# Performance work log

Hardware: AMD Instinct MI355X
Metric: run time of the kernel (lower is better)

Reference implementation:

```python
import jax, jax.numpy as jnp
import numpy as np

B, C, H, W = 8, 384, 128, 128
WSZ = 8          # window size
DH = 32          # dim per head
HEADS = C // DH  # 12
INNER = HEADS * DH
EPS = 1e-5


def setup_inputs() -> dict:
    key = jax.random.key(0)
    ks = jax.random.split(key, 6)
    x = jax.random.normal(ks[0], (B, C, H, W), jnp.float32)
    skip = jax.random.normal(ks[1], (B, C, H, W), jnp.float32)
    # LayerNorm affine params (shape (1, C, 1, 1) in torch; store as (C,))
    g_q = jnp.ones((C,), jnp.float32)
    b_q = jnp.zeros((C,), jnp.float32)
    g_kv = jnp.ones((C,), jnp.float32)
    b_kv = jnp.zeros((C,), jnp.float32)
    # 1x1 conv weights: [out_channels, in_channels]
    Wq = jax.random.normal(ks[2], (INNER, C), jnp.float32) * 0.05
    Wkv = jax.random.normal(ks[3], (2 * INNER, C), jnp.float32) * 0.05
    Wout = jax.random.normal(ks[4], (C, INNER), jnp.float32) * 0.05
    bout = jax.random.normal(ks[5], (C,), jnp.float32) * 0.05
    return dict(x=x, skip=skip, g_q=g_q, b_q=b_q, g_kv=g_kv, b_kv=b_kv,
                Wq=Wq, Wkv=Wkv, Wout=Wout, bout=bout)


def _channel_ln(x, g, b):
    # LayerNorm over channel dim (axis=1), biased variance
    mean = jnp.mean(x, axis=1, keepdims=True)
    var = jnp.mean((x - mean) ** 2, axis=1, keepdims=True)
    return (x - mean) / jnp.sqrt(var + EPS) * g[None, :, None, None] + b[None, :, None, None]


def _to_windows(x):
    # [B, C, H, W] -> [B*nh*nw, C, wsz, wsz]
    b, c, h, w = x.shape
    nh, nw = h // WSZ, w // WSZ
    x = x.reshape(b, c, nh, WSZ, nw, WSZ).transpose(0, 2, 4, 1, 3, 5)
    return x.reshape(b * nh * nw, c, WSZ, WSZ)


def _from_windows(x, b, h, w):
    # [B*nh*nw, C, wsz, wsz] -> [B, C, H, W]
    nh, nw = h // WSZ, w // WSZ
    c = x.shape[1]
    x = x.reshape(b, nh, nw, c, WSZ, WSZ).transpose(0, 3, 1, 4, 2, 5)
    return x.reshape(b, c, h, w)


def _split_heads(t):
    # [Bw, heads*dh, wsz, wsz] -> [Bw, heads, wsz*wsz, dh]
    bw = t.shape[0]
    t = t.reshape(bw, HEADS, DH, WSZ * WSZ)
    return t.transpose(0, 1, 3, 2)


def reference(x, skip, g_q, b_q, g_kv, b_kv, Wq, Wkv, Wout, bout):
    b, _, h, w = x.shape
    xn = _to_windows(_channel_ln(x, g_q, b_q))
    skn = _to_windows(_channel_ln(skip, g_kv, b_kv))
    # 1x1 convs as channel GEMMs
    q = jnp.einsum('oc,bcxy->boxy', Wq, xn)
    kv = jnp.einsum('oc,bcxy->boxy', Wkv, skn)
    k, v = kv[:, :INNER], kv[:, INNER:]
    q, k, v = _split_heads(q), _split_heads(k), _split_heads(v)
    scale = DH ** -0.5
    attn = jax.nn.softmax(jnp.einsum('bhqd,bhkd->bhqk', q, k) * scale, axis=-1)
    out = jnp.einsum('bhqk,bhkd->bhqd', attn, v)
    # [Bw, heads, S, dh] -> [Bw, inner, wsz, wsz]
    out = out.transpose(0, 1, 3, 2).reshape(-1, INNER, WSZ, WSZ)
    out = jnp.einsum('oc,bcxy->boxy', Wout, out) + bout[None, :, None, None]
    return _from_windows(out, b, h, w)
```

## Files before the change

### kernel.cpp

```cpp
#include <hip/hip_runtime.h>
#include <stdint.h>

typedef __attribute__((ext_vector_type(4))) float f32x4;
typedef __attribute__((ext_vector_type(8))) short s16x8;
typedef unsigned int u32;
typedef unsigned short u16;

#define DEVFN static __device__ __forceinline__

constexpr int C = 384;
constexpr int WIMG = 128;
constexpr int HW = 128 * 128;
constexpr float EPS = 1e-5f;
constexpr float QSCALE = 0.17677669529663687f;

constexpr int R1 = 0;
constexpr int R2 = 49152;
constexpr int R3 = 98304;
constexpr int PR = 147456;
constexpr int LDS_BYTES = 163840;

DEVFN u16 f2bf(float f) {
  union { float f; u32 u; } v; v.f = f;
  u32 r = v.u + 0x7fffu + ((v.u >> 16) & 1u);
  return (u16)(r >> 16);
}
DEVFN f32x4 MFMA(s16x8 a, s16x8 b, f32x4 c) {
  return __builtin_amdgcn_mfma_f32_16x16x32_bf16(a, b, c, 0, 0, 0);
}
DEVFN int adr768(int base, int row, int b) { return base + row * 768 + (b ^ ((row & 7) << 4)); }
DEVFN int adr128(int base, int row, int b) { return base + row * 128 + (b ^ ((row & 7) << 4)); }

__global__ void cvt_bf16_kernel(const float* __restrict__ src, u16* __restrict__ dst, int n) {
  int i = (blockIdx.x * blockDim.x + threadIdx.x) * 4;
  if (i + 3 < n) {
    f32x4 v = *(const f32x4*)(src + i);
    u32* d = (u32*)(dst + i);
    d[0] = (u32)f2bf(v[0]) | ((u32)f2bf(v[1]) << 16);
    d[1] = (u32)f2bf(v[2]) | ((u32)f2bf(v[3]) << 16);
  }
}

__global__ void fold_ln_weights(const float* __restrict__ Wq, const float* __restrict__ Wkv,
                                const float* __restrict__ gq, const float* __restrict__ bq,
                                const float* __restrict__ gkv, const float* __restrict__ bkv,
                                u16* __restrict__ wqb, u16* __restrict__ wkb, u16* __restrict__ wvb,
                                float* __restrict__ sg_all, float* __restrict__ sb_all) {
  int r = blockIdx.x * 4 + (threadIdx.x >> 6);
  int lane = threadIdx.x & 63;
  const float* src; const float* g; const float* b; u16* dst; float scale;
  if (r < 384) { src = Wq + (size_t)r * C; g = gq; b = bq; dst = wqb + (size_t)r * C; scale = QSCALE; }
  else {
    src = Wkv + (size_t)(r - 384) * C; g = gkv; b = bkv; scale = 1.f;
    dst = (r < 768) ? wkb + (size_t)(r - 384) * C : wvb + (size_t)(r - 768) * C;
  }
  float sg = 0.f, sb = 0.f;
#pragma unroll
  for (int i = 0; i < 6; ++i) {
    int c = lane + i * 64;
    float wv = src[c], gg = g[c];
    sg += wv * gg; sb += wv * b[c];
    dst[c] = f2bf(wv * gg * scale);
  }
#pragma unroll
  for (int m = 1; m < 64; m <<= 1) { sg += __shfl_xor(sg, m); sb += __shfl_xor(sb, m); }
  if (lane == 0) { sg_all[r] = sg * scale; sb_all[r] = sb * scale; }
}

__launch_bounds__(512, 2)
__global__ void fused_win_attn(
    const float* __restrict__ x, const float* __restrict__ skip,
    const u16* __restrict__ wqb, const u16* __restrict__ wkb,
    const u16* __restrict__ wvb, const u16* __restrict__ wob,
    const float* __restrict__ sg_all, const float* __restrict__ sb_all,
    const float* __restrict__ bout, float* __restrict__ out) {
  extern __shared__ char smem[];
  const int tid = threadIdx.x;
  const int lane = tid & 63;
  const int w = tid >> 6;
  const int l15 = lane & 15;
  const int lg = lane >> 4;
  const int kco = lg * 8;

  const int bid = blockIdx.x;
  const int win = (bid & 7) * 256 + (bid >> 3);
  const int bimg = win >> 8;
  const int Y0 = ((win >> 4) & 15) * 8;
  const int X0 = (win & 15) * 8;
  const size_t img_off = (size_t)bimg * C * HW;

  const f32x4 fzero = {0.f, 0.f, 0.f, 0.f};

  float* red = (float*)(smem + PR);
  float* stats_x = (float*)(smem + PR + 4096);
  float* stats_s = (float*)(smem + PR + 4608);

  const int p = tid & 63;
  const int g8 = tid >> 6;
  const int yy = p >> 3, xx = p & 7;

  for (int tt = 0; tt < 2; ++tt) {
    const float* src = tt ? skip : x;
    const int RB = tt ? R2 : R1;
    const float* gb = src + img_off + (size_t)(Y0 + yy) * WIMG + X0 + xx;
    float s = 0.f, q = 0.f;
#pragma unroll
    for (int i = 0; i < 24; ++i) {
      int c0 = g8 * 48 + i * 2;
      float v0 = gb[(size_t)c0 * HW];
      float v1 = gb[(size_t)c0 * HW + HW];
      s += v0 + v1; q += v0 * v0 + v1 * v1;
      *(u32*)(smem + adr768(RB, p, c0 * 2)) = (u32)f2bf(v0) | ((u32)f2bf(v1) << 16);
    }
    red[tid * 2] = s; red[tid * 2 + 1] = q;
    __syncthreads();
    if (tid < 64) {
      float sm = 0.f, sq = 0.f;
#pragma unroll
      for (int gg = 0; gg < 8; ++gg) { sm += red[(gg * 64 + tid) * 2]; sq += red[(gg * 64 + tid) * 2 + 1]; }
      float mean = sm * (1.f / 384.f);
      float var = sq * (1.f / 384.f) - mean * mean;
      float* st = tt ? stats_s : stats_x;
      st[tid * 2] = mean; st[tid * 2 + 1] = 1.f / sqrtf(var + EPS);
    }
    __syncthreads();
  }

  {
    f32x4 acc[3][4];
#pragma unroll
    for (int nn = 0; nn < 3; ++nn)
#pragma unroll
      for (int m = 0; m < 4; ++m) acc[nn][m] = fzero;
#pragma unroll
    for (int k = 0; k < 12; ++k) {
      s16x8 A[4];
#pragma unroll
      for (int m = 0; m < 4; ++m)
        A[m] = *(const s16x8*)(smem + adr768(R2, m * 16 + l15, (k * 32 + kco) * 2));
#pragma unroll
      for (int nn = 0; nn < 3; ++nn) {
        s16x8 B = *(const s16x8*)(wkb + (size_t)((3 * w + nn) * 16 + l15) * C + k * 32 + kco);
#pragma unroll
        for (int m = 0; m < 4; ++m) acc[nn][m] = MFMA(A[m], B, acc[nn][m]);
      }
    }
#pragma unroll
    for (int nn = 0; nn < 3; ++nn) {
      int o = (3 * w + nn) * 16 + l15;
      float sg = sg_all[384 + o], sb = sb_all[384 + o];
#pragma unroll
      for (int m = 0; m < 4; ++m)
#pragma unroll
        for (int j = 0; j < 4; ++j) {
          int tok = m * 16 + lg * 4 + j;
          float mn = stats_s[tok * 2], rs = stats_s[tok * 2 + 1];
          *(u16*)(smem + adr768(R3, tok, o * 2)) = f2bf(rs * acc[nn][m][j] - rs * mn * sg + sb);
        }
    }
  }

  f32x4 accV[3][4];
  {
#pragma unroll
    for (int mm = 0; mm < 3; ++mm)
#pragma unroll
      for (int n = 0; n < 4; ++n) accV[mm][n] = fzero;
#pragma unroll
    for (int k = 0; k < 12; ++k) {
      s16x8 Bv[4];
#pragma unroll
      for (int n = 0; n < 4; ++n)
        Bv[n] = *(const s16x8*)(smem + adr768(R2, n * 16 + l15, (k * 32 + kco) * 2));
#pragma unroll
      for (int mm = 0; mm < 3; ++mm) {
        s16x8 A = *(const s16x8*)(wvb + (size_t)((3 * w + mm) * 16 + l15) * C + k * 32 + kco);
#pragma unroll
        for (int n = 0; n < 4; ++n) accV[mm][n] = MFMA(A, Bv[n], accV[mm][n]);
      }
    }
  }

  f32x4 accQ[3][4];
  {
#pragma unroll
    for (int nn = 0; nn < 3; ++nn)
#pragma unroll
      for (int m = 0; m < 4; ++m) accQ[nn][m] = fzero;
#pragma unroll
    for (int k = 0; k < 12; ++k) {
      s16x8 A[4];
#pragma unroll
      for (int m = 0; m < 4; ++m)
        A[m] = *(const s16x8*)(smem + adr768(R1, m * 16 + l15, (k * 32 + kco) * 2));
#pragma unroll
      for (int nn = 0; nn < 3; ++nn) {
        s16x8 B = *(const s16x8*)(wqb + (size_t)((3 * w + nn) * 16 + l15) * C + k * 32 + kco);
#pragma unroll
        for (int m = 0; m < 4; ++m) accQ[nn][m] = MFMA(A[m], B, accQ[nn][m]);
      }
    }
  }
  __syncthreads();

  {
#pragma unroll
    for (int mm = 0; mm < 3; ++mm)
#pragma unroll
      for (int j = 0; j < 4; ++j) {
        int dh = (3 * w + mm) * 16 + lg * 4 + j;
        float sg = sg_all[768 + dh], sb = sb_all[768 + dh];
#pragma unroll
        for (int n = 0; n < 4; ++n) {
          int tok = n * 16 + l15;
          float mn = stats_s[tok * 2], rs = stats_s[tok * 2 + 1];
          *(u16*)(smem + adr128(R2, dh, tok * 2)) = f2bf(rs * accV[mm][n][j] - rs * mn * sg + sb);
        }
      }
#pragma unroll
    for (int nn = 0; nn < 3; ++nn) {
      int o = (3 * w + nn) * 16 + l15;
      float sg = sg_all[o], sb = sb_all[o];
#pragma unroll
      for (int m = 0; m < 4; ++m)
#pragma unroll
        for (int j = 0; j < 4; ++j) {
          int tok = m * 16 + lg * 4 + j;
          float mn = stats_x[tok * 2], rs = stats_x[tok * 2 + 1];
          *(u16*)(smem + adr768(R1, tok, o * 2)) = f2bf(rs * accQ[nn][m][j] - rs * mn * sg + sb);
        }
    }
  }
  __syncthreads();

  const int qt = w & 3;
  const int hh = w >> 2;
  char* strip = smem + PR + w * 2048;
  const int swzq = (l15 & 7) << 4;

  s16x8 oA[6];

#pragma unroll
  for (int hloc = 0; hloc < 6; ++hloc) {
    const int h = hh * 6 + hloc;
    s16x8 bq = *(const s16x8*)(smem + adr768(R1, qt * 16 + l15, h * 64 + lg * 16));
    f32x4 sc[4];
#pragma unroll
    for (int m = 0; m < 4; ++m) {
      s16x8 ak = *(const s16x8*)(smem + adr768(R3, m * 16 + l15, h * 64 + lg * 16));
      sc[m] = MFMA(ak, bq, fzero);
    }
    float mx = sc[0][0];
#pragma unroll
    for (int m = 0; m < 4; ++m)
#pragma unroll
      for (int j = 0; j < 4; ++j) mx = fmaxf(mx, sc[m][j]);
    mx = fmaxf(mx, __shfl_xor(mx, 16));
    mx = fmaxf(mx, __shfl_xor(mx, 32));
    float ex[4][4];
    float sum = 0.f;
#pragma unroll
    for (int m = 0; m < 4; ++m)
#pragma unroll
      for (int j = 0; j < 4; ++j) { float e = __expf(sc[m][j] - mx); ex[m][j] = e; sum += e; }
    sum += __shfl_xor(sum, 16);
    sum += __shfl_xor(sum, 32);
    float inv = 1.0f / sum;
#pragma unroll
    for (int m = 0; m < 4; ++m)
#pragma unroll
      for (int j2 = 0; j2 < 2; ++j2) {
        u32 pk = (u32)f2bf(ex[m][2 * j2] * inv) | ((u32)f2bf(ex[m][2 * j2 + 1] * inv) << 16);
        *(u32*)(strip + l15 * 128 + ((m * 32 + lg * 8 + j2 * 4) ^ swzq)) = pk;
      }
    f32x4 ov[2] = {fzero, fzero};
#pragma unroll
    for (int ks = 0; ks < 2; ++ks) {
      s16x8 ap = *(const s16x8*)(strip + l15 * 128 + ((ks * 64 + lg * 16) ^ swzq));
#pragma unroll
      for (int n = 0; n < 2; ++n) {
        s16x8 bv = *(const s16x8*)(smem + adr128(R2, h * 32 + n * 16 + l15, ks * 64 + lg * 16));
        ov[n] = MFMA(ap, bv, ov[n]);
      }
    }
#pragma unroll
    for (int n = 0; n < 2; ++n)
#pragma unroll
      for (int j = 0; j < 4; ++j) {
        int row = lg * 4 + j;
        *(u16*)(strip + row * 128 + ((n * 32 + l15 * 2) ^ ((row & 7) << 4))) = f2bf(ov[n][j]);
      }
    oA[hloc] = *(const s16x8*)(strip + l15 * 128 + ((lg * 16) ^ swzq));
  }

#pragma unroll
  for (int hloc = 0; hloc < 6; ++hloc)
    *(s16x8*)(smem + adr768(R1, qt * 16 + l15, (hh * 6 + hloc) * 64 + lg * 16)) = oA[hloc];
  __syncthreads();

  f32x4 outacc[3][4];
#pragma unroll
  for (int nn = 0; nn < 3; ++nn)
#pragma unroll
    for (int m = 0; m < 4; ++m) outacc[nn][m] = fzero;
#pragma unroll
  for (int k = 0; k < 12; ++k) {
    s16x8 A[4];
#pragma unroll
    for (int m = 0; m < 4; ++m)
      A[m] = *(const s16x8*)(smem + adr768(R1, m * 16 + l15, (k * 32 + kco) * 2));
#pragma unroll
    for (int nn = 0; nn < 3; ++nn) {
      s16x8 B = *(const s16x8*)(wob + (size_t)((3 * w + nn) * 16 + l15) * C + k * 32 + kco);
#pragma unroll
      for (int m = 0; m < 4; ++m) outacc[nn][m] = MFMA(A[m], B, outacc[nn][m]);
    }
  }
  __syncthreads();

  float* outf = (float*)smem;
#pragma unroll
  for (int nn = 0; nn < 3; ++nn) {
    int o = (3 * w + nn) * 16 + l15;
    float bo = bout[o];
#pragma unroll
    for (int m = 0; m < 4; ++m)
#pragma unroll
      for (int j = 0; j < 4; ++j)
        outf[(m * 16 + lg * 4 + j) * 385 + o] = outacc[nn][m][j] + bo;
  }
  __syncthreads();
  {
    float* ob = out + img_off + (size_t)(Y0 + yy) * WIMG + X0 + xx;
#pragma unroll
    for (int i = 0; i < 48; ++i) {
      int c = g8 * 48 + i;
      ob[(size_t)c * HW] = outf[p * 385 + c];
    }
  }
}

extern "C" void kernel_launch(void* const* d_in, const int* in_sizes, int n_in,
                              void* d_out, int out_size, void* d_ws, size_t ws_size,
                              hipStream_t stream) {
  const float* x    = (const float*)d_in[0];
  const float* skip = (const float*)d_in[1];
  const float* gq   = (const float*)d_in[2];
  const float* bq   = (const float*)d_in[3];
  const float* gkv  = (const float*)d_in[4];
  const float* bkv  = (const float*)d_in[5];
  const float* Wq   = (const float*)d_in[6];
  const float* Wkv  = (const float*)d_in[7];
  const float* Wout = (const float*)d_in[8];
  const float* bout = (const float*)d_in[9];
  float* out = (float*)d_out;

  char* ws = (char*)d_ws;
  u16* wqb = (u16*)(ws);
  u16* wkb = (u16*)(ws + 294912);
  u16* wvb = (u16*)(ws + 589824);
  u16* wob = (u16*)(ws + 884736);
  float* sg_all = (float*)(ws + 1179648);
  float* sb_all = (float*)(ws + 1184256);

  hipFuncSetAttribute((const void*)fused_win_attn,
                      hipFuncAttributeMaxDynamicSharedMemorySize, LDS_BYTES);

  fold_ln_weights<<<288, 256, 0, stream>>>(Wq, Wkv, gq, bq, gkv, bkv, wqb, wkb, wvb, sg_all, sb_all);
  cvt_bf16_kernel<<<144, 256, 0, stream>>>(Wout, wob, 147456);

  fused_win_attn<<<2048, 512, LDS_BYTES, stream>>>(
      x, skip, wqb, wkb, wvb, wob, sg_all, sb_all, bout, out);
}
```

Measured before the change: 599.1 us.

## Double block to 1024 threads and redistribute K/Q/V/attention/output work across 16 waves

The fused window-attention kernel now runs 16 waves per block instead of 8. The K and Q projections run concurrently on separate wave halves, and the V projection and output GEMM are split over token halves. Attention now handles 3 heads per wave, with a smaller per-wave strip, and writes its output directly into the Q region instead of staging it through registers. The aim is more latency hiding and per-block parallelism, at the cost of extra barriers and possibly lower occupancy, since the LDS budget still limits how many blocks fit per CU.

```diff
diff --git a/kernel.cpp b/kernel.cpp
--- a/kernel.cpp
+++ b/kernel.cpp
@@ -67,7 +67,7 @@
   if (lane == 0) { sg_all[r] = sg * scale; sb_all[r] = sb * scale; }
 }
 
-__launch_bounds__(512, 2)
+__launch_bounds__(1024, 4)
 __global__ void fused_win_attn(
     const float* __restrict__ x, const float* __restrict__ skip,
     const u16* __restrict__ wqb, const u16* __restrict__ wkb,
@@ -79,8 +79,8 @@
   const int lane = tid & 63;
   const int w = tid >> 6;
   const int l15 = lane & 15;
-  const int lg = lane >> 4;
-  const int kco = lg * 8;
+  const int g = lane >> 4;
+  const int kco = g * 8;
 
   const int bid = blockIdx.x;
   const int win = (bid & 7) * 256 + (bid >> 3);
@@ -92,11 +92,10 @@
   const f32x4 fzero = {0.f, 0.f, 0.f, 0.f};
 
   float* red = (float*)(smem + PR);
-  float* stats_x = (float*)(smem + PR + 4096);
-  float* stats_s = (float*)(smem + PR + 4608);
-
-  const int p = tid & 63;
-  const int g8 = tid >> 6;
+  float* stats_x = (float*)(smem + PR + 8192);
+  float* stats_s = (float*)(smem + PR + 8704);
+
+  const int p = lane;
   const int yy = p >> 3, xx = p & 7;
 
   for (int tt = 0; tt < 2; ++tt) {
@@ -105,8 +104,8 @@
     const float* gb = src + img_off + (size_t)(Y0 + yy) * WIMG + X0 + xx;
     float s = 0.f, q = 0.f;
 #pragma unroll
-    for (int i = 0; i < 24; ++i) {
-      int c0 = g8 * 48 + i * 2;
+    for (int i = 0; i < 12; ++i) {
+      int c0 = w * 24 + i * 2;
       float v0 = gb[(size_t)c0 * HW];
       float v1 = gb[(size_t)c0 * HW + HW];
       s += v0 + v1; q += v0 * v0 + v1 * v1;
@@ -117,7 +116,7 @@
     if (tid < 64) {
       float sm = 0.f, sq = 0.f;
 #pragma unroll
-      for (int gg = 0; gg < 8; ++gg) { sm += red[(gg * 64 + tid) * 2]; sq += red[(gg * 64 + tid) * 2 + 1]; }
+      for (int gg = 0; gg < 16; ++gg) { sm += red[(gg * 64 + tid) * 2]; sq += red[(gg * 64 + tid) * 2 + 1]; }
       float mean = sm * (1.f / 384.f);
       float var = sq * (1.f / 384.f) - mean * mean;
       float* st = tt ? stats_s : stats_x;
@@ -126,7 +125,8 @@
     __syncthreads();
   }
 
-  {
+  f32x4 accQ[3][4];
+  if (w < 8) {
     f32x4 acc[3][4];
 #pragma unroll
     for (int nn = 0; nn < 3; ++nn)
@@ -137,7 +137,7 @@
       s16x8 A[4];
 #pragma unroll
       for (int m = 0; m < 4; ++m)
-        A[m] = *(const s16x8*)(smem + adr768(R2, m * 16 + l15, (k * 32 + kco) * 2));
+        A[m] = *(const s16x8*)(smem + adr768(R2, m * 16 + l15, k * 64 + g * 16));
 #pragma unroll
       for (int nn = 0; nn < 3; ++nn) {
         s16x8 B = *(const s16x8*)(wkb + (size_t)((3 * w + nn) * 16 + l15) * C + k * 32 + kco);
@@ -153,36 +153,13 @@
       for (int m = 0; m < 4; ++m)
 #pragma unroll
         for (int j = 0; j < 4; ++j) {
-          int tok = m * 16 + lg * 4 + j;
+          int tok = m * 16 + g * 4 + j;
           float mn = stats_s[tok * 2], rs = stats_s[tok * 2 + 1];
           *(u16*)(smem + adr768(R3, tok, o * 2)) = f2bf(rs * acc[nn][m][j] - rs * mn * sg + sb);
         }
     }
-  }
-
-  f32x4 accV[3][4];
-  {
-#pragma unroll
-    for (int mm = 0; mm < 3; ++mm)
-#pragma unroll
-      for (int n = 0; n < 4; ++n) accV[mm][n] = fzero;
-#pragma unroll
-    for (int k = 0; k < 12; ++k) {
-      s16x8 Bv[4];
-#pragma unroll
-      for (int n = 0; n < 4; ++n)
-        Bv[n] = *(const s16x8*)(smem + adr768(R2, n * 16 + l15, (k * 32 + kco) * 2));
-#pragma unroll
-      for (int mm = 0; mm < 3; ++mm) {
-        s16x8 A = *(const s16x8*)(wvb + (size_t)((3 * w + mm) * 16 + l15) * C + k * 32 + kco);
-#pragma unroll
-        for (int n = 0; n < 4; ++n) accV[mm][n] = MFMA(A, Bv[n], accV[mm][n]);
-      }
-    }
-  }
-
-  f32x4 accQ[3][4];
-  {
+  } else {
+    const int wq = w - 8;
 #pragma unroll
     for (int nn = 0; nn < 3; ++nn)
 #pragma unroll
@@ -192,10 +169,10 @@
       s16x8 A[4];
 #pragma unroll
       for (int m = 0; m < 4; ++m)
-        A[m] = *(const s16x8*)(smem + adr768(R1, m * 16 + l15, (k * 32 + kco) * 2));
+        A[m] = *(const s16x8*)(smem + adr768(R1, m * 16 + l15, k * 64 + g * 16));
 #pragma unroll
       for (int nn = 0; nn < 3; ++nn) {
-        s16x8 B = *(const s16x8*)(wqb + (size_t)((3 * w + nn) * 16 + l15) * C + k * 32 + kco);
+        s16x8 B = *(const s16x8*)(wqb + (size_t)((3 * wq + nn) * 16 + l15) * C + k * 32 + kco);
 #pragma unroll
         for (int m = 0; m < 4; ++m) accQ[nn][m] = MFMA(A[m], B, accQ[nn][m]);
       }
@@ -203,138 +180,164 @@
   }
   __syncthreads();
 
-  {
-#pragma unroll
-    for (int mm = 0; mm < 3; ++mm)
-#pragma unroll
-      for (int j = 0; j < 4; ++j) {
-        int dh = (3 * w + mm) * 16 + lg * 4 + j;
-        float sg = sg_all[768 + dh], sb = sb_all[768 + dh];
-#pragma unroll
-        for (int n = 0; n < 4; ++n) {
-          int tok = n * 16 + l15;
-          float mn = stats_s[tok * 2], rs = stats_s[tok * 2 + 1];
-          *(u16*)(smem + adr128(R2, dh, tok * 2)) = f2bf(rs * accV[mm][n][j] - rs * mn * sg + sb);
-        }
-      }
+  if (w >= 8) {
+    const int wq = w - 8;
 #pragma unroll
     for (int nn = 0; nn < 3; ++nn) {
-      int o = (3 * w + nn) * 16 + l15;
+      int o = (3 * wq + nn) * 16 + l15;
       float sg = sg_all[o], sb = sb_all[o];
 #pragma unroll
       for (int m = 0; m < 4; ++m)
 #pragma unroll
         for (int j = 0; j < 4; ++j) {
-          int tok = m * 16 + lg * 4 + j;
+          int tok = m * 16 + g * 4 + j;
           float mn = stats_x[tok * 2], rs = stats_x[tok * 2 + 1];
           *(u16*)(smem + adr768(R1, tok, o * 2)) = f2bf(rs * accQ[nn][m][j] - rs * mn * sg + sb);
         }
     }
   }
-  __syncthreads();
-
-  const int qt = w & 3;
-  const int hh = w >> 2;
-  char* strip = smem + PR + w * 2048;
-  const int swzq = (l15 & 7) << 4;
-
-  s16x8 oA[6];
-
-#pragma unroll
-  for (int hloc = 0; hloc < 6; ++hloc) {
-    const int h = hh * 6 + hloc;
-    s16x8 bq = *(const s16x8*)(smem + adr768(R1, qt * 16 + l15, h * 64 + lg * 16));
-    f32x4 sc[4];
-#pragma unroll
-    for (int m = 0; m < 4; ++m) {
-      s16x8 ak = *(const s16x8*)(smem + adr768(R3, m * 16 + l15, h * 64 + lg * 16));
-      sc[m] = MFMA(ak, bq, fzero);
-    }
-    float mx = sc[0][0];
-#pragma unroll
-    for (int m = 0; m < 4; ++m)
-#pragma unroll
-      for (int j = 0; j < 4; ++j) mx = fmaxf(mx, sc[m][j]);
-    mx = fmaxf(mx, __shfl_xor(mx, 16));
-    mx = fmaxf(mx, __shfl_xor(mx, 32));
-    float ex[4][4];
-    float sum = 0.f;
-#pragma unroll
-    for (int m = 0; m < 4; ++m)
-#pragma unroll
-      for (int j = 0; j < 4; ++j) { float e = __expf(sc[m][j] - mx); ex[m][j] = e; sum += e; }
-    sum += __shfl_xor(sum, 16);
-    sum += __shfl_xor(sum, 32);
-    float inv = 1.0f / sum;
-#pragma unroll
-    for (int m = 0; m < 4; ++m)
-#pragma unroll
-      for (int j2 = 0; j2 < 2; ++j2) {
-        u32 pk = (u32)f2bf(ex[m][2 * j2] * inv) | ((u32)f2bf(ex[m][2 * j2 + 1] * inv) << 16);
-        *(u32*)(strip + l15 * 128 + ((m * 32 + lg * 8 + j2 * 4) ^ swzq)) = pk;
-      }
-    f32x4 ov[2] = {fzero, fzero};
-#pragma unroll
-    for (int ks = 0; ks < 2; ++ks) {
-      s16x8 ap = *(const s16x8*)(strip + l15 * 128 + ((ks * 64 + lg * 16) ^ swzq));
-#pragma unroll
-      for (int n = 0; n < 2; ++n) {
-        s16x8 bv = *(const s16x8*)(smem + adr128(R2, h * 32 + n * 16 + l15, ks * 64 + lg * 16));
-        ov[n] = MFMA(ap, bv, ov[n]);
-      }
-    }
-#pragma unroll
-    for (int n = 0; n < 2; ++n)
-#pragma unroll
-      for (int j = 0; j < 4; ++j) {
-        int row = lg * 4 + j;
-        *(u16*)(strip + row * 128 + ((n * 32 + l15 * 2) ^ ((row & 7) << 4))) = f2bf(ov[n][j]);
-      }
-    oA[hloc] = *(const s16x8*)(strip + l15 * 128 + ((lg * 16) ^ swzq));
-  }
-
-#pragma unroll
-  for (int hloc = 0; hloc < 6; ++hloc)
-    *(s16x8*)(smem + adr768(R1, qt * 16 + l15, (hh * 6 + hloc) * 64 + lg * 16)) = oA[hloc];
-  __syncthreads();
-
-  f32x4 outacc[3][4];
-#pragma unroll
-  for (int nn = 0; nn < 3; ++nn)
-#pragma unroll
-    for (int m = 0; m < 4; ++m) outacc[nn][m] = fzero;
-#pragma unroll
-  for (int k = 0; k < 12; ++k) {
-    s16x8 A[4];
-#pragma unroll
-    for (int m = 0; m < 4; ++m)
-      A[m] = *(const s16x8*)(smem + adr768(R1, m * 16 + l15, (k * 32 + kco) * 2));
+  f32x4 accV[3][2];
+  {
+    const int mg = w & 7, nh = w >> 3;
+#pragma unroll
+    for (int mm = 0; mm < 3; ++mm)
+#pragma unroll
+      for (int n = 0; n < 2; ++n) accV[mm][n] = fzero;
+#pragma unroll
+    for (int k = 0; k < 12; ++k) {
+      s16x8 Bv[2];
+#pragma unroll
+      for (int n = 0; n < 2; ++n)
+        Bv[n] = *(const s16x8*)(smem + adr768(R2, (2 * nh + n) * 16 + l15, k * 64 + g * 16));
+#pragma unroll
+      for (int mm = 0; mm < 3; ++mm) {
+        s16x8 A = *(const s16x8*)(wvb + (size_t)((3 * mg + mm) * 16 + l15) * C + k * 32 + kco);
+#pragma unroll
+        for (int n = 0; n < 2; ++n) accV[mm][n] = MFMA(A, Bv[n], accV[mm][n]);
+      }
+    }
+  }
+  __syncthreads();
+
+  {
+    const int mg = w & 7, nh = w >> 3;
+#pragma unroll
+    for (int n = 0; n < 2; ++n) {
+      int tok = (2 * nh + n) * 16 + l15;
+      float mn = stats_s[tok * 2], rs = stats_s[tok * 2 + 1];
+#pragma unroll
+      for (int mm = 0; mm < 3; ++mm)
+#pragma unroll
+        for (int j = 0; j < 4; ++j) {
+          int dh = (3 * mg + mm) * 16 + g * 4 + j;
+          float sg = sg_all[768 + dh], sb = sb_all[768 + dh];
+          *(u16*)(smem + adr128(R2, dh, tok * 2)) = f2bf(rs * accV[mm][n][j] - rs * mn * sg + sb);
+        }
+    }
+  }
+  __syncthreads();
+
+  {
+    const int qt = w & 3, hq = w >> 2;
+    char* strip = smem + PR + w * 1024;
+    const int swz = (l15 & 3) << 4;
+
+#pragma unroll
+    for (int hloc = 0; hloc < 3; ++hloc) {
+      const int h = hq * 3 + hloc;
+      s16x8 bq = *(const s16x8*)(smem + adr768(R1, qt * 16 + l15, h * 64 + g * 16));
+      f32x4 sc[4];
+#pragma unroll
+      for (int m = 0; m < 4; ++m) {
+        s16x8 ak = *(const s16x8*)(smem + adr768(R3, m * 16 + l15, h * 64 + g * 16));
+        sc[m] = MFMA(ak, bq, fzero);
+      }
+      float mx = sc[0][0];
+#pragma unroll
+      for (int m = 0; m < 4; ++m)
+#pragma unroll
+        for (int j = 0; j < 4; ++j) mx = fmaxf(mx, sc[m][j]);
+      mx = fmaxf(mx, __shfl_xor(mx, 16));
+      mx = fmaxf(mx, __shfl_xor(mx, 32));
+      float ex[4][4];
+      float sum = 0.f;
+#pragma unroll
+      for (int m = 0; m < 4; ++m)
+#pragma unroll
+        for (int j = 0; j < 4; ++j) { float e = __expf(sc[m][j] - mx); ex[m][j] = e; sum += e; }
+      sum += __shfl_xor(sum, 16);
+      sum += __shfl_xor(sum, 32);
+      float inv = 1.0f / sum;
+      f32x4 ov[2] = {fzero, fzero};
+#pragma unroll
+      for (int ks = 0; ks < 2; ++ks) {
+#pragma unroll
+        for (int mm = 0; mm < 2; ++mm)
+#pragma unroll
+          for (int j2 = 0; j2 < 2; ++j2) {
+            u32 pk = (u32)f2bf(ex[2 * ks + mm][2 * j2] * inv) |
+                     ((u32)f2bf(ex[2 * ks + mm][2 * j2 + 1] * inv) << 16);
+            *(u32*)(strip + l15 * 64 + ((mm * 32 + g * 8 + j2 * 4) ^ swz)) = pk;
+          }
+        s16x8 ap = *(const s16x8*)(strip + l15 * 64 + ((g * 16) ^ swz));
+#pragma unroll
+        for (int n = 0; n < 2; ++n) {
+          s16x8 bv = *(const s16x8*)(smem + adr128(R2, h * 32 + n * 16 + l15, ks * 64 + g * 16));
+          ov[n] = MFMA(ap, bv, ov[n]);
+        }
+      }
+#pragma unroll
+      for (int n = 0; n < 2; ++n)
+#pragma unroll
+        for (int j = 0; j < 4; ++j)
+          *(u16*)(smem + adr768(R1, qt * 16 + g * 4 + j, (h * 32 + n * 16 + l15) * 2)) = f2bf(ov[n][j]);
+    }
+  }
+  __syncthreads();
+
+  f32x4 oacc[3][2];
+  {
+    const int mh = w >> 3, ng = w & 7;
+#pragma unroll
+    for (int nn = 0; nn < 3; ++nn)
+#pragma unroll
+      for (int m = 0; m < 2; ++m) oacc[nn][m] = fzero;
+#pragma unroll
+    for (int k = 0; k < 12; ++k) {
+      s16x8 A[2];
+#pragma unroll
+      for (int m = 0; m < 2; ++m)
+        A[m] = *(const s16x8*)(smem + adr768(R1, (2 * mh + m) * 16 + l15, k * 64 + g * 16));
+#pragma unroll
+      for (int nn = 0; nn < 3; ++nn) {
+        s16x8 B = *(const s16x8*)(wob + (size_t)((3 * ng + nn) * 16 + l15) * C + k * 32 + kco);
+#pragma unroll
+        for (int m = 0; m < 2; ++m) oacc[nn][m] = MFMA(A[m], B, oacc[nn][m]);
+      }
+    }
+  }
+  __syncthreads();
+
+  float* outf = (float*)smem;
+  {
+    const int mh = w >> 3, ng = w & 7;
 #pragma unroll
     for (int nn = 0; nn < 3; ++nn) {
-      s16x8 B = *(const s16x8*)(wob + (size_t)((3 * w + nn) * 16 + l15) * C + k * 32 + kco);
-#pragma unroll
-      for (int m = 0; m < 4; ++m) outacc[nn][m] = MFMA(A[m], B, outacc[nn][m]);
-    }
-  }
-  __syncthreads();
-
-  float* outf = (float*)smem;
-#pragma unroll
-  for (int nn = 0; nn < 3; ++nn) {
-    int o = (3 * w + nn) * 16 + l15;
-    float bo = bout[o];
-#pragma unroll
-    for (int m = 0; m < 4; ++m)
-#pragma unroll
-      for (int j = 0; j < 4; ++j)
-        outf[(m * 16 + lg * 4 + j) * 385 + o] = outacc[nn][m][j] + bo;
+      int o = (3 * ng + nn) * 16 + l15;
+      float bo = bout[o];
+#pragma unroll
+      for (int m = 0; m < 2; ++m)
+#pragma unroll
+        for (int j = 0; j < 4; ++j)
+          outf[((2 * mh + m) * 16 + g * 4 + j) * 385 + o] = oacc[nn][m][j] + bo;
+    }
   }
   __syncthreads();
   {
     float* ob = out + img_off + (size_t)(Y0 + yy) * WIMG + X0 + xx;
 #pragma unroll
-    for (int i = 0; i < 48; ++i) {
-      int c = g8 * 48 + i;
+    for (int i = 0; i < 24; ++i) {
+      int c = w * 24 + i;
       ob[(size_t)c * HW] = outf[p * 385 + c];
     }
   }
@@ -369,6 +372,6 @@
   fold_ln_weights<<<288, 256, 0, stream>>>(Wq, Wkv, gq, bq, gkv, bkv, wqb, wkb, wvb, sg_all, sb_all);
   cvt_bf16_kernel<<<144, 256, 0, stream>>>(Wout, wob, 147456);
 
-  fused_win_attn<<<2048, 512, LDS_BYTES, stream>>>(
+  fused_win_attn<<<2048, 1024, LDS_BYTES, stream>>>(
       x, skip, wqb, wkb, wvb, wob, sg_all, sb_all, bout, out);
 }
```

Result: slower. 723.4 us (+20.7%).
